# Optimization experiments

Hardware: AMD Instinct MI355X
Metric: run time of the kernel (lower is better)

Reference implementation:

```python
import jax, jax.numpy as jnp
import numpy as np
from jax import lax

N = 50000      # total nodes
E = 400000     # total edges
F = 512        # input feature dim
B = 50         # graphs in batch
NP = 1000      # nodes per graph
OUT = 10       # out_channel
EPS = 1e-5


def setup_inputs():
    key = jax.random.key(0)
    ks = jax.random.split(key, 20)
    x = jax.random.normal(ks[0], (N, F), jnp.float32)
    eg = jnp.arange(E) // (E // B)                       # graph id per edge
    src = jax.random.randint(ks[1], (E,), 0, NP) + eg * NP
    dst = jax.random.randint(ks[2], (E,), 0, NP) + eg * NP
    edge_index = jnp.stack([src, dst]).astype(jnp.int32)
    batch = (jnp.arange(N) // NP).astype(jnp.int32)
    s = 0.02
    W1 = s * jax.random.normal(ks[3], (1024, F), jnp.float32)
    b1 = jnp.zeros((1024,), jnp.float32)
    g1 = jnp.ones((1024,), jnp.float32)
    be1 = jnp.zeros((1024,), jnp.float32)
    Wp = s * jax.random.normal(ks[4], (1, 2 * 1024), jnp.float32)  # EdgePooling lin
    bp = jnp.zeros((1,), jnp.float32)
    W2 = s * jax.random.normal(ks[5], (512, 1024), jnp.float32)
    b2 = jnp.zeros((512,), jnp.float32)
    g2 = jnp.ones((512,), jnp.float32)
    be2 = jnp.zeros((512,), jnp.float32)
    Wfc = s * jax.random.normal(ks[6], (200, 512), jnp.float32)
    bfc = jnp.zeros((200,), jnp.float32)
    Wfc1 = s * jax.random.normal(ks[7], (OUT, 200), jnp.float32)
    bfc1 = jnp.zeros((OUT,), jnp.float32)
    return dict(x=x, edge_index=edge_index, batch=batch, W1=W1, b1=b1, g1=g1,
                be1=be1, Wp=Wp, bp=bp, W2=W2, b2=b2, g2=g2, be2=be2,
                Wfc=Wfc, bfc=bfc, Wfc1=Wfc1, bfc1=bfc1)


def _bn(h, g, b):
    m = h.mean(0)
    v = jnp.var(h, axis=0)  # biased var, as torch BatchNorm1d (train mode)
    return (h - m) * (g / jnp.sqrt(v + EPS)) + b


def _edge_pool(h, src, dst, batch, Wp, bp):
    # raw edge score: Linear([h_src || h_dst]) -> scalar per edge
    e = jnp.concatenate([h[src], h[dst]], axis=-1) @ Wp.T + bp  # [E,1]
    e = e[:, 0]
    # softmax over edges sharing the same destination node (PyG default)
    m = jax.ops.segment_max(e, dst, num_segments=N)
    ex = jnp.exp(e - m[dst])
    den = jax.ops.segment_sum(ex, dst, num_segments=N)
    score = ex / den[dst] + 0.5  # add_to_edge_score = 0.5

    # greedy contraction in descending-score order (sequential, like PyG)
    order = jnp.argsort(-score)
    so, do = src[order], dst[order]

    def step(merged, sd):
        s_, d_ = sd
        ok = (~merged[s_]) & (~merged[d_])
        merged = merged.at[s_].set(merged[s_] | ok)
        merged = merged.at[d_].set(merged[d_] | ok)
        return merged, ok

    _, valid = lax.scan(step, jnp.zeros(N, bool), (so, do))
    ec = (jnp.cumsum(valid.astype(jnp.int32)) - 1)      # cluster id per contracted edge
    num_merged = valid.astype(jnp.int32).sum()

    OOB = jnp.int32(N)
    cluster = jnp.full((N,), -1, jnp.int32)
    cluster = cluster.at[jnp.where(valid, so, OOB)].set(ec, mode='drop')
    cluster = cluster.at[jnp.where(valid, do, OOB)].set(ec, mode='drop')
    unmerged = cluster < 0
    rank = jnp.cumsum(unmerged.astype(jnp.int32)) - 1
    cluster = jnp.where(unmerged, num_merged + rank, cluster)

    # per-cluster multiplier: contracted-edge score, 1.0 for singleton nodes
    mult = jnp.ones((N,), h.dtype)
    mult = mult.at[jnp.where(valid, ec, OOB)].set(score[order], mode='drop')

    new_x = jax.ops.segment_sum(h, cluster, num_segments=N) * mult[:, None]
    new_batch = jnp.full((N,), B, jnp.int32).at[cluster].set(batch)  # pad slots -> dummy graph B
    return new_x, new_batch


def reference(x, edge_index, batch, W1, b1, g1, be1, Wp, bp, W2, b2, g2, be2,
              Wfc, bfc, Wfc1, bfc1):
    src, dst = edge_index[0], edge_index[1]
    # ChebConv K=1 == plain linear (only T_0 = x term)
    h = jax.nn.relu(_bn(x @ W1.T + b1, g1, be1))         # [N,1024]
    h, nb = _edge_pool(h, src, dst, batch, Wp, bp)       # [N,1024] padded, [N]
    h = jax.nn.relu(_bn(h @ W2.T + b2, g2, be2))         # [N,512]
    # global mean pool over graphs (dummy segment B holds padding)
    sums = jax.ops.segment_sum(h, nb, num_segments=B + 1)[:B]
    cnt = jax.ops.segment_sum(jnp.ones((N,), h.dtype), nb, num_segments=B + 1)[:B]
    pooled = sums / jnp.maximum(cnt, 1.0)[:, None]       # [B,512]
    hid = jax.nn.relu(pooled @ Wfc.T + bfc)              # [B,200]; dropout is eval no-op
    return hid @ Wfc1.T + bfc1                           # [B,OUT]
```

## Files before the change

### kernel.cpp

```cpp
#include <hip/hip_runtime.h>

#define Nn   50000
#define Ee   400000
#define Ff   512
#define H1   1024
#define H2   512
#define Bb   50
#define OUTd 10
#define EPSc 1e-5f
#define NPg  1000
#define EPg  8000

typedef _Float16 h8 __attribute__((ext_vector_type(8)));
typedef _Float16 h4 __attribute__((ext_vector_type(4)));
typedef float f4 __attribute__((ext_vector_type(4)));

__device__ __forceinline__ unsigned fmap(float f) {
    unsigned u = __float_as_uint(f);
    return (u & 0x80000000u) ? ~u : (u | 0x80000000u);
}
__device__ __forceinline__ float funmap(unsigned m) {
    unsigned u = (m & 0x80000000u) ? (m ^ 0x80000000u) : ~m;
    return __uint_as_float(u);
}

__device__ __forceinline__ void gl_lds16(const void* g, void* l) {
    __builtin_amdgcn_global_load_lds(
        (const __attribute__((address_space(1))) unsigned int*)g,
        (__attribute__((address_space(3))) unsigned int*)l,
        16, 0, 0);
}

__global__ void init_kernel(double* cs1, double* css1, double* cs2, double* css2, int* scal) {
    int i = blockIdx.x * blockDim.x + threadIdx.x;
    int nth = gridDim.x * blockDim.x;
    for (int j = i; j < H1; j += nth) { cs1[j] = 0.0; css1[j] = 0.0; }
    for (int j = i; j < H2; j += nth) { cs2[j] = 0.0; css2[j] = 0.0; }
    if (i < 16) scal[i] = 0;
}

__global__ void prep_kernel(const float* __restrict__ x, _Float16* __restrict__ xhi, _Float16* __restrict__ xlo,
                            const float* __restrict__ W1, _Float16* __restrict__ w1h, _Float16* __restrict__ w1l,
                            const float* __restrict__ W2, _Float16* __restrict__ w2h) {
    int i = blockIdx.x * blockDim.x + threadIdx.x;
    int nth = gridDim.x * blockDim.x;
    const int nx = Nn * Ff / 4, nw1 = H1 * Ff / 4, nw2 = H2 * H1 / 4;
    for (int k = i; k < nx; k += nth) {
        float4 v = ((const float4*)x)[k];
        h4 H = { (_Float16)v.x, (_Float16)v.y, (_Float16)v.z, (_Float16)v.w };
        h4 L = { (_Float16)(v.x - (float)H[0]), (_Float16)(v.y - (float)H[1]),
                 (_Float16)(v.z - (float)H[2]), (_Float16)(v.w - (float)H[3]) };
        ((h4*)xhi)[k] = H;
        ((h4*)xlo)[k] = L;
    }
    for (int k = i; k < nw1; k += nth) {
        float4 v = ((const float4*)W1)[k];
        h4 H = { (_Float16)v.x, (_Float16)v.y, (_Float16)v.z, (_Float16)v.w };
        h4 L = { (_Float16)(v.x - (float)H[0]), (_Float16)(v.y - (float)H[1]),
                 (_Float16)(v.z - (float)H[2]), (_Float16)(v.w - (float)H[3]) };
        ((h4*)w1h)[k] = H;
        ((h4*)w1l)[k] = L;
    }
    for (int k = i; k < nw2; k += nth) {
        float4 v = ((const float4*)W2)[k];
        h4 H = { (_Float16)v.x, (_Float16)v.y, (_Float16)v.z, (_Float16)v.w };
        ((h4*)w2h)[k] = H;
    }
}

__global__ __launch_bounds__(512) void gemm1_256_kernel(
        const _Float16* __restrict__ Ahi, const _Float16* __restrict__ Alo,
        const _Float16* __restrict__ Bhi, const _Float16* __restrict__ Blo,
        const float* __restrict__ bias, float* __restrict__ C,
        double* __restrict__ csum, double* __restrict__ cssum)
{
    const int M = Nn;
    const int nwg = gridDim.x, orig = blockIdx.x;
    const int qq = nwg >> 3, rr = nwg & 7;
    const int xcd = orig & 7, idx = orig >> 3;
    const int lin = (xcd < rr ? xcd * (qq + 1) : rr * (qq + 1) + (xcd - rr) * qq) + idx;
    const int nT = H1 / 256;
    const int bmI = lin / nT;
    const int bm = bmI * 256, bn = (lin - bmI * nT) * 256;
    __shared__ __align__(16) _Float16 smem[2][2][256 * 32];
    const int tid = threadIdx.x, lane = tid & 63, wave = tid >> 6;
    const int rIn = lane >> 2;
    const int kSrcByte = ((((lane & 3) - ((lane >> 3) & 3)) & 3) << 4);
    const int wr = wave >> 2, wc = wave & 3;
    const int lr = lane & 15, kb = lane >> 4;
    const int pGr = ((kb + ((lr >> 1) & 3)) & 3) << 3;
    const int sArr = wave >> 2;
    const int sQtr = wave & 3;
    const _Float16* sGp = sArr ? Alo : Ahi;
    f4 acc[8][4] = {};

    auto STAGE = [&](int b, int k0) {
        _Float16* lp = smem[b][sArr] + sQtr * (64 * 32);
#pragma unroll
        for (int c2 = 0; c2 < 4; ++c2) {
            int row = min(bm + sQtr * 64 + c2 * 16 + rIn, M - 1);
            gl_lds16((const char*)sGp + ((size_t)row * Ff + k0) * 2 + kSrcByte, lp + c2 * 512);
        }
    };

    int cur = 0;
    STAGE(0, 0);
    for (int k0 = 0; k0 < Ff; k0 += 32) {
        __syncthreads();
        if (k0 + 32 < Ff) STAGE(cur ^ 1, k0 + 32);
        const _Float16* AhP = smem[cur][0];
        const _Float16* AlP = smem[cur][1];
        h8 ahf[8], alf[8];
#pragma unroll
        for (int mi = 0; mi < 8; ++mi) {
            const int ar = (wr * 128 + mi * 16 + lr) * 32 + pGr;
            ahf[mi] = *(const h8*)&AhP[ar];
            alf[mi] = *(const h8*)&AlP[ar];
        }
#pragma unroll
        for (int ni = 0; ni < 4; ++ni) {
            const size_t boff = (size_t)(bn + wc * 64 + ni * 16 + lr) * Ff + k0 + kb * 8;
            const h8 bh = *(const h8*)&Bhi[boff];
            const h8 bl = *(const h8*)&Blo[boff];
#pragma unroll
            for (int mi = 0; mi < 8; ++mi) {
                acc[mi][ni] = __builtin_amdgcn_mfma_f32_16x16x32_f16(ahf[mi], bh, acc[mi][ni], 0, 0, 0);
                acc[mi][ni] = __builtin_amdgcn_mfma_f32_16x16x32_f16(ahf[mi], bl, acc[mi][ni], 0, 0, 0);
                acc[mi][ni] = __builtin_amdgcn_mfma_f32_16x16x32_f16(alf[mi], bh, acc[mi][ni], 0, 0, 0);
            }
        }
        cur ^= 1;
    }
#pragma unroll
    for (int ni = 0; ni < 4; ++ni) {
        const int col = bn + wc * 64 + ni * 16 + lr;
        const float bv = bias[col];
        double sd_ = 0.0, ssd = 0.0;
#pragma unroll
        for (int mi = 0; mi < 8; ++mi)
#pragma unroll
            for (int r = 0; r < 4; ++r) {
                int row = bm + wr * 128 + mi * 16 + kb * 4 + r;
                if (row < M) {
                    float v = acc[mi][ni][r] + bv;
                    C[(size_t)row * H1 + col] = v;
                    sd_ += (double)v;
                    ssd += (double)v * (double)v;
                }
            }
        sd_ += __shfl_xor(sd_, 16); ssd += __shfl_xor(ssd, 16);
        sd_ += __shfl_xor(sd_, 32); ssd += __shfl_xor(ssd, 32);
        if (kb == 0) {
            atomicAdd(&csum[col], sd_);
            atomicAdd(&cssum[col], ssd);
        }
    }
}

__global__ __launch_bounds__(256) void gemm2_kernel(
        const _Float16* __restrict__ Ag, const _Float16* __restrict__ Bh,
        const float* __restrict__ bias, float* __restrict__ C,
        const int* __restrict__ Mptr, int nT,
        double* __restrict__ csum, double* __restrict__ cssum)
{
    const int M = Mptr[0];
    const int nwg = gridDim.x, orig = blockIdx.x;
    const int qq = nwg >> 3, rr = nwg & 7;
    const int xcd = orig & 7, idx = orig >> 3;
    const int lin = (xcd < rr ? xcd * (qq + 1) : rr * (qq + 1) + (xcd - rr) * qq) + idx;
    const int bmI = lin / nT;
    const int bm = bmI * 128, bn = (lin - bmI * nT) * 128;
    if (bm >= M) return;
    __shared__ __align__(16) _Float16 smem[2][128 * 32];
    const int tid = threadIdx.x, lane = tid & 63, wave = tid >> 6;
    const int rIn = lane >> 2;
    const int kSrcByte = ((((lane & 3) - ((lane >> 3) & 3)) & 3) << 4);
    const int wr = wave >> 1, wc = wave & 1;
    const int lr = lane & 15, kb = lane >> 4;
    const int pGr = ((kb + ((lr >> 1) & 3)) & 3) << 3;
    f4 acc[4][4] = {};

    auto STAGE = [&](int b, int k0) {
        _Float16* lp = smem[b] + wave * (32 * 32);
#pragma unroll
        for (int c2 = 0; c2 < 2; ++c2) {
            int row = min(bm + wave * 32 + c2 * 16 + rIn, M - 1);
            gl_lds16((const char*)Ag + ((size_t)row * H1 + k0) * 2 + kSrcByte, lp + c2 * 512);
        }
    };

    int cur = 0;
    STAGE(0, 0);
    for (int k0 = 0; k0 < H1; k0 += 32) {
        __syncthreads();
        if (k0 + 32 < H1) STAGE(cur ^ 1, k0 + 32);
        const _Float16* AhP = smem[cur];
        h8 ahf[4];
#pragma unroll
        for (int mi = 0; mi < 4; ++mi)
            ahf[mi] = *(const h8*)&AhP[(wr * 64 + mi * 16 + lr) * 32 + pGr];
#pragma unroll
        for (int ni = 0; ni < 4; ++ni) {
            const h8 bh = *(const h8*)&Bh[(size_t)(bn + wc * 64 + ni * 16 + lr) * H1 + k0 + kb * 8];
#pragma unroll
            for (int mi = 0; mi < 4; ++mi)
                acc[mi][ni] = __builtin_amdgcn_mfma_f32_16x16x32_f16(ahf[mi], bh, acc[mi][ni], 0, 0, 0);
        }
        cur ^= 1;
    }
#pragma unroll
    for (int ni = 0; ni < 4; ++ni) {
        const int col = bn + wc * 64 + ni * 16 + lr;
        const float bv = bias[col];
        double sd_ = 0.0, ssd = 0.0;
#pragma unroll
        for (int mi = 0; mi < 4; ++mi)
#pragma unroll
            for (int r = 0; r < 4; ++r) {
                int row = bm + wr * 64 + mi * 16 + kb * 4 + r;
                if (row < M) {
                    float v = acc[mi][ni][r] + bv;
                    C[(size_t)row * H2 + col] = v;
                    sd_ += (double)v;
                    ssd += (double)v * (double)v;
                }
            }
        sd_ += __shfl_xor(sd_, 16); ssd += __shfl_xor(ssd, 16);
        sd_ += __shfl_xor(sd_, 32); ssd += __shfl_xor(ssd, 32);
        if (kb == 0) {
            atomicAdd(&csum[col], sd_);
            atomicAdd(&cssum[col], ssd);
        }
    }
}

__global__ void bnparam_kernel(const double* __restrict__ s, const double* __restrict__ ss,
                               const float* __restrict__ g, const float* __restrict__ be,
                               float* __restrict__ a, float* __restrict__ bb, int cols,
                               const float* __restrict__ padBias, const int* __restrict__ CvPtr) {
    int j = blockIdx.x * blockDim.x + threadIdx.x;
    if (j >= cols) return;
    double sum = s[j], sumsq = ss[j];
    if (CvPtr) {
        double pad = (double)(Nn - CvPtr[0]);
        double bv = padBias ? (double)padBias[j] : 0.0;
        sum += pad * bv; sumsq += pad * bv * bv;
    }
    double mean = sum / (double)Nn;
    double var = sumsq / (double)Nn - mean * mean;
    float aj = g[j] / sqrtf((float)var + EPSc);
    a[j] = aj;
    bb[j] = be[j] - (float)mean * aj;
}

__global__ __launch_bounds__(256) void pq_kernel(const float* __restrict__ h,
        const float* __restrict__ a, const float* __restrict__ bb,
        const float* __restrict__ Wp, float* __restrict__ p, float* __restrict__ q) {
    const int n = blockIdx.x * 4 + (threadIdx.x >> 6);
    if (n >= Nn) return;
    const int lane = threadIdx.x & 63;
    float sp = 0.f, sq = 0.f;
    const float* row = h + (size_t)n * H1;
#pragma unroll
    for (int u = 0; u < 4; ++u) {
        int j = u * 256 + lane * 4;
        float4 v = *(const float4*)(row + j);
        const float4 av = *(const float4*)(a + j);
        const float4 bv = *(const float4*)(bb + j);
        v.x = fmaxf(v.x * av.x + bv.x, 0.f);
        v.y = fmaxf(v.y * av.y + bv.y, 0.f);
        v.z = fmaxf(v.z * av.z + bv.z, 0.f);
        v.w = fmaxf(v.w * av.w + bv.w, 0.f);
        const float4 wp = *(const float4*)(Wp + j);
        const float4 wq = *(const float4*)(Wp + H1 + j);
        sp += v.x * wp.x + v.y * wp.y + v.z * wp.z + v.w * wp.w;
        sq += v.x * wq.x + v.y * wq.y + v.z * wq.z + v.w * wq.w;
    }
#pragma unroll
    for (int off = 32; off > 0; off >>= 1) {
        sp += __shfl_xor(sp, off);
        sq += __shfl_xor(sq, off);
    }
    if (lane == 0) { p[n] = sp; q[n] = sq; }
}

__global__ __launch_bounds__(1024) void match_fused_kernel(
        const int* __restrict__ ei,
        const float* __restrict__ p, const float* __restrict__ q,
        const float* __restrict__ bp,
        unsigned long long* __restrict__ packed,
        int* __restrict__ nodeA, int* __restrict__ nodeB,
        float* __restrict__ multc, int* __restrict__ scal,
        int* __restrict__ gbase, int* __restrict__ gcnt) {
    __shared__ __align__(16) char LB[52096];
    unsigned short* lst = (unsigned short*)LB;
    float* earr = (float*)LB;
    float* pl = (float*)(LB + 32000);
    float* ql = pl + NPg;
    unsigned long long* best = (unsigned long long*)(LB + 32000);
    unsigned* maxu = (unsigned*)(LB + 40000);
    int* mergedS = (int*)(LB + 40000);
    unsigned long long* den = (unsigned long long*)(LB + 44000);
    float* lmult = (float*)(LB + 44000);
    unsigned short* lsA = (unsigned short*)(LB + 48000);
    unsigned short* ldA = (unsigned short*)(LB + 50000);
    int* cnts = (int*)(LB + 52032);

    const int g = blockIdx.x;
    const int tid = threadIdx.x;
    const int e0 = g * EPg, n0 = g * NPg;
    const int* srcp = ei + e0;
    const int* dstp = ei + Ee + e0;
    const float bpv = bp[0];

    for (int i = tid; i < NPg; i += 1024) {
        pl[i] = p[n0 + i];
        ql[i] = q[n0 + i];
        maxu[i] = 0u;
        den[i] = 0ull;
    }
    __syncthreads();
    for (int i = tid; i < EPg; i += 1024) {
        int s = srcp[i] - n0, d = dstp[i] - n0;
        float e = pl[s] + ql[d] + bpv;
        earr[i] = e;
        atomicMax(&maxu[d], fmap(e));
    }
    __syncthreads();
    for (int i = tid; i < EPg; i += 1024) {
        int d = dstp[i] - n0;
        float ex = expf(earr[i] - funmap(maxu[d]));
        atomicAdd(&den[d], (unsigned long long)(ex * 4294967296.0f));
    }
    __syncthreads();
    for (int i = tid; i < EPg; i += 1024) {
        int s = srcp[i] - n0, d = dstp[i] - n0;
        float ex = expf(earr[i] - funmap(maxu[d]));
        float den_f = (float)((double)den[d] * (1.0 / 4294967296.0));
        float sc = ex / den_f + 0.5f;
        packed[e0 + i] = ((unsigned long long)__float_as_uint(sc) << 33)
                       | ((unsigned long long)(8191u - (unsigned)i) << 20)
                       | ((unsigned long long)(unsigned)s << 10) | (unsigned long long)(unsigned)d;
    }
    __syncthreads();
    for (int i = tid; i < NPg; i += 1024) mergedS[i] = 0;
    for (int i = tid; i < EPg; i += 1024) lst[i] = (unsigned short)i;
    if (tid == 0) { cnts[0] = EPg; cnts[1] = 0; cnts[2] = 0; }
    __syncthreads();
    int cur = 0;
    for (int round = 0; round < 20000; ++round) {
        const int n_cur = cnts[cur];
        if (n_cur == 0) break;
        if (tid == 0) cnts[cur ^ 1] = 0;
        for (int i = tid; i < NPg; i += 1024) best[i] = 0ull;
        __syncthreads();
        for (int ii = tid; ii < n_cur; ii += 1024) {
            int le = lst[cur * EPg + ii];
            unsigned long long pk = packed[e0 + le];
            int s = (int)((pk >> 10) & 1023), d = (int)(pk & 1023);
            if (mergedS[s] | mergedS[d]) { lst[cur * EPg + ii] = 0xFFFF; continue; }
            atomicMax(&best[s], pk);
            atomicMax(&best[d], pk);
        }
        __syncthreads();
        for (int ii = tid; ii < n_cur; ii += 1024) {
            int le = lst[cur * EPg + ii];
            if (le == 0xFFFF) continue;
            unsigned long long pk = packed[e0 + le];
            int s = (int)((pk >> 10) & 1023), d = (int)(pk & 1023);
            if (best[s] == pk && best[d] == pk) {
                int c = atomicAdd(&cnts[2], 1);
                lsA[c] = (unsigned short)s;
                ldA[c] = (s == d) ? (unsigned short)0xFFFF : (unsigned short)d;
                lmult[c] = __uint_as_float((unsigned)(pk >> 33));
                mergedS[s] = 1;
                if (d != s) mergedS[d] = 1;
            } else {
                int pos = atomicAdd(&cnts[cur ^ 1], 1);
                lst[(cur ^ 1) * EPg + pos] = (unsigned short)le;
            }
        }
        __syncthreads();
        cur ^= 1;
    }
    for (int i = tid; i < NPg; i += 1024) {
        if (!mergedS[i]) {
            int c = atomicAdd(&cnts[2], 1);
            lsA[c] = (unsigned short)i;
            ldA[c] = 0xFFFF;
            lmult[c] = 1.0f;
        }
    }
    __syncthreads();
    if (tid == 0) {
        int ncl = cnts[2];
        int base = atomicAdd(&scal[2], ncl);
        cnts[3] = base;
        gbase[g] = base;
        gcnt[g] = ncl;
    }
    __syncthreads();
    const int ncl = cnts[2], base = cnts[3];
    for (int i = tid; i < ncl; i += 1024) {
        nodeA[base + i] = n0 + (int)lsA[i];
        nodeB[base + i] = (ldA[i] == 0xFFFF) ? -1 : (n0 + (int)ldA[i]);
        multc[base + i] = lmult[i];
    }
}

__global__ __launch_bounds__(256) void gather_kernel(const float* __restrict__ h,
        const float* __restrict__ a, const float* __restrict__ bb,
        const int* __restrict__ nodeA, const int* __restrict__ nodeB,
        const float* __restrict__ multc, const int* __restrict__ scal,
        _Float16* __restrict__ Ag) {
    int c = blockIdx.x * 4 + (threadIdx.x >> 6);
    if (c >= scal[2]) return;
    const int lane = threadIdx.x & 63;
    int na = nodeA[c], nb = nodeB[c];
    float mu = multc[c];
#pragma unroll
    for (int u = 0; u < 4; ++u) {
        int j = u * 256 + lane * 4;
        const float4 av = *(const float4*)(a + j);
        const float4 bv = *(const float4*)(bb + j);
        float4 v = *(const float4*)(h + (size_t)na * H1 + j);
        v.x = fmaxf(v.x * av.x + bv.x, 0.f);
        v.y = fmaxf(v.y * av.y + bv.y, 0.f);
        v.z = fmaxf(v.z * av.z + bv.z, 0.f);
        v.w = fmaxf(v.w * av.w + bv.w, 0.f);
        if (nb >= 0) {
            float4 w = *(const float4*)(h + (size_t)nb * H1 + j);
            v.x += fmaxf(w.x * av.x + bv.x, 0.f);
            v.y += fmaxf(w.y * av.y + bv.y, 0.f);
            v.z += fmaxf(w.z * av.z + bv.z, 0.f);
            v.w += fmaxf(w.w * av.w + bv.w, 0.f);
        }
        h4 o = { (_Float16)(mu * v.x), (_Float16)(mu * v.y), (_Float16)(mu * v.z), (_Float16)(mu * v.w) };
        *(h4*)(Ag + (size_t)c * H1 + j) = o;
    }
}

__global__ __launch_bounds__(256) void pool_seg_kernel(const float* __restrict__ C2,
        const float* __restrict__ a2, const float* __restrict__ bb2,
        const int* __restrict__ gbase, const int* __restrict__ gcnt,
        float* __restrict__ pool) {
    const int g = blockIdx.x;
    const int j = blockIdx.y * 256 + threadIdx.x;
    const int b0 = gbase[g], cN = gcnt[g];
    const float aj = a2[j], bj = bb2[j];
    float s = 0.f;
    for (int c = b0; c < b0 + cN; ++c)
        s += fmaxf(C2[(size_t)c * H2 + j] * aj + bj, 0.f);
    pool[g * H2 + j] = s;
}

__global__ void fc1_kernel(const float* __restrict__ pool, const int* __restrict__ gcnt,
                           const float* __restrict__ Wfc, const float* __restrict__ bfc,
                           float* __restrict__ hid) {
    int g = blockIdx.x;
    int o = threadIdx.x;
    float inv = 1.0f / fmaxf((float)gcnt[g], 1.0f);
    if (o < 200) {
        float s = 0.f;
        for (int j = 0; j < H2; ++j) s += (pool[g * H2 + j] * inv) * Wfc[o * H2 + j];
        hid[g * 200 + o] = fmaxf(s + bfc[o], 0.f);
    }
}
__global__ void fc2_kernel(const float* __restrict__ hid, const float* __restrict__ Wfc1,
                           const float* __restrict__ bfc1, float* __restrict__ out) {
    int idx = threadIdx.x;
    if (idx < Bb * OUTd) {
        int g = idx / OUTd, o = idx % OUTd;
        float s = bfc1[o];
        for (int t = 0; t < 200; ++t) s += hid[g * 200 + t] * Wfc1[o * 200 + t];
        out[idx] = s;
    }
}

extern "C" void kernel_launch(void* const* d_in, const int* in_sizes, int n_in,
                              void* d_out, int out_size, void* d_ws, size_t ws_size,
                              hipStream_t stream) {
    (void)in_sizes; (void)n_in; (void)out_size; (void)ws_size;
    const float* x    = (const float*)d_in[0];
    const int*   ei   = (const int*)d_in[1];
    const float* W1   = (const float*)d_in[3];
    const float* b1   = (const float*)d_in[4];
    const float* g1   = (const float*)d_in[5];
    const float* be1  = (const float*)d_in[6];
    const float* Wp   = (const float*)d_in[7];
    const float* bp   = (const float*)d_in[8];
    const float* W2   = (const float*)d_in[9];
    const float* b2   = (const float*)d_in[10];
    const float* g2   = (const float*)d_in[11];
    const float* be2  = (const float*)d_in[12];
    const float* Wfc  = (const float*)d_in[13];
    const float* bfc  = (const float*)d_in[14];
    const float* Wfc1 = (const float*)d_in[15];
    const float* bfc1 = (const float*)d_in[16];

    char* w = (char*)d_ws;
    auto take = [&](size_t bytes) -> char* {
        char* r = w;
        w += (bytes + 255) & ~(size_t)255;
        return r;
    };
    float* h      = (float*)take((size_t)Nn * H1 * 4);
    _Float16* xhi = (_Float16*)take((size_t)Nn * Ff * 2);
    _Float16* xlo = (_Float16*)take((size_t)Nn * Ff * 2);
    _Float16* w1h = (_Float16*)take((size_t)H1 * Ff * 2);
    _Float16* w1l = (_Float16*)take((size_t)H1 * Ff * 2);
    _Float16* w2h = (_Float16*)take((size_t)H2 * H1 * 2);
    float* p      = (float*)take((size_t)Nn * 4);
    float* q      = (float*)take((size_t)Nn * 4);
    unsigned long long* packed = (unsigned long long*)take((size_t)Ee * 8);
    int* nodeA    = (int*)take((size_t)Nn * 4);
    int* nodeB    = (int*)take((size_t)Nn * 4);
    float* multc  = (float*)take((size_t)Nn * 4);
    double* cs1   = (double*)take((size_t)H1 * 8);
    double* css1  = (double*)take((size_t)H1 * 8);
    double* cs2   = (double*)take((size_t)H2 * 8);
    double* css2  = (double*)take((size_t)H2 * 8);
    float* a1     = (float*)take((size_t)H1 * 4);
    float* bb1    = (float*)take((size_t)H1 * 4);
    float* a2     = (float*)take((size_t)H2 * 4);
    float* bb2    = (float*)take((size_t)H2 * 4);
    float* pool   = (float*)take((size_t)Bb * H2 * 4);
    float* hid    = (float*)take((size_t)Bb * 200 * 4);
    int* scal     = (int*)take(64 * 4);
    int* gbase    = (int*)take(64 * 4);
    int* gcnt     = (int*)take(64 * 4);
    _Float16* Ag  = xhi;
    float* C2o    = h;

    const int mT  = (Nn + 127) / 128;
    const int mT2 = (Nn + 255) / 256;

    init_kernel<<<dim3(16), dim3(256), 0, stream>>>(cs1, css1, cs2, css2, scal);
    prep_kernel<<<dim3(2048), dim3(256), 0, stream>>>(x, xhi, xlo, W1, w1h, w1l, W2, w2h);
    gemm1_256_kernel<<<dim3(mT2 * (H1 / 256)), dim3(512), 0, stream>>>(
        xhi, xlo, w1h, w1l, b1, h, cs1, css1);
    bnparam_kernel<<<dim3((H1 + 255) / 256), dim3(256), 0, stream>>>(cs1, css1, g1, be1, a1, bb1, H1, (const float*)nullptr, (const int*)nullptr);
    pq_kernel<<<dim3((Nn + 3) / 4), dim3(256), 0, stream>>>(h, a1, bb1, Wp, p, q);
    match_fused_kernel<<<dim3(Bb), dim3(1024), 0, stream>>>(ei, p, q, bp, packed,
        nodeA, nodeB, multc, scal, gbase, gcnt);
    gather_kernel<<<dim3((Nn + 3) / 4), dim3(256), 0, stream>>>(h, a1, bb1, nodeA, nodeB, multc, scal, Ag);
    gemm2_kernel<<<dim3(mT * (H2 / 128)), dim3(256), 0, stream>>>(
        Ag, w2h, b2, C2o, scal + 2, H2 / 128, cs2, css2);
    bnparam_kernel<<<dim3((H2 + 255) / 256), dim3(256), 0, stream>>>(cs2, css2, g2, be2, a2, bb2, H2, b2, scal + 2);
    pool_seg_kernel<<<dim3(Bb, H2 / 256), dim3(256), 0, stream>>>(C2o, a2, bb2, gbase, gcnt, pool);
    fc1_kernel<<<dim3(Bb), dim3(256), 0, stream>>>(pool, gcnt, Wfc, bfc, hid);
    fc2_kernel<<<dim3(1), dim3(512), 0, stream>>>(hid, Wfc1, bfc1, (float*)d_out);
}
```

Measured before the change: 795.5 us.

## Stage B operand tiles in LDS for both GEMMs and fuse init into prep

Both GEMM kernels now load the weight (B) tiles into shared memory through async global-to-LDS copies, using the same swizzled layout as the A tiles. Previously every wave read B fragments straight from global memory, once per k-step. This cuts redundant global traffic and latency stalls inside the MFMA loop. The cost is more LDS: gemm1 goes to 128KB of shared memory, which may reduce occupancy. The accumulator-zeroing init kernel is also folded into prep_kernel, saving one launch.

Result: faster. 666.8 us (-16.2%).

```diff
diff --git a/kernel.cpp b/kernel.cpp
--- a/kernel.cpp
+++ b/kernel.cpp
@@ -31,19 +31,16 @@
         16, 0, 0);
 }
 
-__global__ void init_kernel(double* cs1, double* css1, double* cs2, double* css2, int* scal) {
+__global__ void prep_kernel(const float* __restrict__ x, _Float16* __restrict__ xhi, _Float16* __restrict__ xlo,
+                            const float* __restrict__ W1, _Float16* __restrict__ w1h, _Float16* __restrict__ w1l,
+                            const float* __restrict__ W2, _Float16* __restrict__ w2h,
+                            double* __restrict__ cs1, double* __restrict__ css1,
+                            double* __restrict__ cs2, double* __restrict__ css2, int* __restrict__ scal) {
     int i = blockIdx.x * blockDim.x + threadIdx.x;
     int nth = gridDim.x * blockDim.x;
     for (int j = i; j < H1; j += nth) { cs1[j] = 0.0; css1[j] = 0.0; }
     for (int j = i; j < H2; j += nth) { cs2[j] = 0.0; css2[j] = 0.0; }
     if (i < 16) scal[i] = 0;
-}
-
-__global__ void prep_kernel(const float* __restrict__ x, _Float16* __restrict__ xhi, _Float16* __restrict__ xlo,
-                            const float* __restrict__ W1, _Float16* __restrict__ w1h, _Float16* __restrict__ w1l,
-                            const float* __restrict__ W2, _Float16* __restrict__ w2h) {
-    int i = blockIdx.x * blockDim.x + threadIdx.x;
-    int nth = gridDim.x * blockDim.x;
     const int nx = Nn * Ff / 4, nw1 = H1 * Ff / 4, nw2 = H2 * H1 / 4;
     for (int k = i; k < nx; k += nth) {
         float4 v = ((const float4*)x)[k];
@@ -82,24 +79,27 @@
     const int nT = H1 / 256;
     const int bmI = lin / nT;
     const int bm = bmI * 256, bn = (lin - bmI * nT) * 256;
-    __shared__ __align__(16) _Float16 smem[2][2][256 * 32];
+    __shared__ __align__(16) _Float16 smem[2][4][256 * 32];
     const int tid = threadIdx.x, lane = tid & 63, wave = tid >> 6;
     const int rIn = lane >> 2;
     const int kSrcByte = ((((lane & 3) - ((lane >> 3) & 3)) & 3) << 4);
     const int wr = wave >> 2, wc = wave & 3;
     const int lr = lane & 15, kb = lane >> 4;
     const int pGr = ((kb + ((lr >> 1) & 3)) & 3) << 3;
-    const int sArr = wave >> 2;
-    const int sQtr = wave & 3;
-    const _Float16* sGp = sArr ? Alo : Ahi;
+    const int arr = wave >> 1;
+    const int hv = wave & 1;
+    const bool isA = (arr < 2);
+    const _Float16* gp = (arr == 0) ? Ahi : (arr == 1) ? Alo : (arr == 2) ? Bhi : Blo;
+    const int tb = isA ? bm : bn;
     f4 acc[8][4] = {};
 
     auto STAGE = [&](int b, int k0) {
-        _Float16* lp = smem[b][sArr] + sQtr * (64 * 32);
-#pragma unroll
-        for (int c2 = 0; c2 < 4; ++c2) {
-            int row = min(bm + sQtr * 64 + c2 * 16 + rIn, M - 1);
-            gl_lds16((const char*)sGp + ((size_t)row * Ff + k0) * 2 + kSrcByte, lp + c2 * 512);
+        _Float16* lp = smem[b][arr] + hv * (128 * 32);
+#pragma unroll
+        for (int c = 0; c < 8; ++c) {
+            int row = tb + hv * 128 + c * 16 + rIn;
+            if (isA) row = min(row, M - 1);
+            gl_lds16((const char*)gp + ((size_t)row * Ff + k0) * 2 + kSrcByte, lp + c * 512);
         }
     };
 
@@ -110,6 +110,8 @@
         if (k0 + 32 < Ff) STAGE(cur ^ 1, k0 + 32);
         const _Float16* AhP = smem[cur][0];
         const _Float16* AlP = smem[cur][1];
+        const _Float16* BhP = smem[cur][2];
+        const _Float16* BlP = smem[cur][3];
         h8 ahf[8], alf[8];
 #pragma unroll
         for (int mi = 0; mi < 8; ++mi) {
@@ -119,9 +121,9 @@
         }
 #pragma unroll
         for (int ni = 0; ni < 4; ++ni) {
-            const size_t boff = (size_t)(bn + wc * 64 + ni * 16 + lr) * Ff + k0 + kb * 8;
-            const h8 bh = *(const h8*)&Bhi[boff];
-            const h8 bl = *(const h8*)&Blo[boff];
+            const int br = (wc * 64 + ni * 16 + lr) * 32 + pGr;
+            const h8 bh = *(const h8*)&BhP[br];
+            const h8 bl = *(const h8*)&BlP[br];
 #pragma unroll
             for (int mi = 0; mi < 8; ++mi) {
                 acc[mi][ni] = __builtin_amdgcn_mfma_f32_16x16x32_f16(ahf[mi], bh, acc[mi][ni], 0, 0, 0);
@@ -171,7 +173,7 @@
     const int bmI = lin / nT;
     const int bm = bmI * 128, bn = (lin - bmI * nT) * 128;
     if (bm >= M) return;
-    __shared__ __align__(16) _Float16 smem[2][128 * 32];
+    __shared__ __align__(16) _Float16 smem[2][2][128 * 32];
     const int tid = threadIdx.x, lane = tid & 63, wave = tid >> 6;
     const int rIn = lane >> 2;
     const int kSrcByte = ((((lane & 3) - ((lane >> 3) & 3)) & 3) << 4);
@@ -181,11 +183,17 @@
     f4 acc[4][4] = {};
 
     auto STAGE = [&](int b, int k0) {
-        _Float16* lp = smem[b] + wave * (32 * 32);
-#pragma unroll
-        for (int c2 = 0; c2 < 2; ++c2) {
-            int row = min(bm + wave * 32 + c2 * 16 + rIn, M - 1);
-            gl_lds16((const char*)Ag + ((size_t)row * H1 + k0) * 2 + kSrcByte, lp + c2 * 512);
+        const bool isA = (wave < 2);
+        const _Float16* gp = isA ? Ag : Bh;
+        _Float16* lp = smem[b][isA ? 0 : 1];
+        const int tb = isA ? bm : bn;
+        const int hf = wave & 1;
+#pragma unroll
+        for (int c2 = 0; c2 < 4; ++c2) {
+            int c = hf * 4 + c2;
+            int row = tb + c * 16 + rIn;
+            if (isA) row = min(row, M - 1);
+            gl_lds16((const char*)gp + ((size_t)row * H1 + k0) * 2 + kSrcByte, lp + c * 512);
         }
     };
 
@@ -194,18 +202,21 @@
     for (int k0 = 0; k0 < H1; k0 += 32) {
         __syncthreads();
         if (k0 + 32 < H1) STAGE(cur ^ 1, k0 + 32);
-        const _Float16* AhP = smem[cur];
-        h8 ahf[4];
+        const _Float16* AhP = smem[cur][0];
+        const _Float16* BhP = smem[cur][1];
+        const int ar = (wr * 64 + lr) * 32 + pGr;
+        const int br = (wc * 64 + lr) * 32 + pGr;
+        h8 ahf[4], bhf[4];
+#pragma unroll
+        for (int i = 0; i < 4; ++i) {
+            ahf[i] = *(const h8*)&AhP[ar + i * 512];
+            bhf[i] = *(const h8*)&BhP[br + i * 512];
+        }
 #pragma unroll
         for (int mi = 0; mi < 4; ++mi)
-            ahf[mi] = *(const h8*)&AhP[(wr * 64 + mi * 16 + lr) * 32 + pGr];
-#pragma unroll
-        for (int ni = 0; ni < 4; ++ni) {
-            const h8 bh = *(const h8*)&Bh[(size_t)(bn + wc * 64 + ni * 16 + lr) * H1 + k0 + kb * 8];
-#pragma unroll
-            for (int mi = 0; mi < 4; ++mi)
-                acc[mi][ni] = __builtin_amdgcn_mfma_f32_16x16x32_f16(ahf[mi], bh, acc[mi][ni], 0, 0, 0);
-        }
+#pragma unroll
+            for (int ni = 0; ni < 4; ++ni)
+                acc[mi][ni] = __builtin_amdgcn_mfma_f32_16x16x32_f16(ahf[mi], bhf[ni], acc[mi][ni], 0, 0, 0);
         cur ^= 1;
     }
 #pragma unroll
@@ -535,8 +546,8 @@
     const int mT  = (Nn + 127) / 128;
     const int mT2 = (Nn + 255) / 256;
 
-    init_kernel<<<dim3(16), dim3(256), 0, stream>>>(cs1, css1, cs2, css2, scal);
-    prep_kernel<<<dim3(2048), dim3(256), 0, stream>>>(x, xhi, xlo, W1, w1h, w1l, W2, w2h);
+    prep_kernel<<<dim3(2048), dim3(256), 0, stream>>>(x, xhi, xlo, W1, w1h, w1l, W2, w2h,
+                                                      cs1, css1, cs2, css2, scal);
     gemm1_256_kernel<<<dim3(mT2 * (H1 / 256)), dim3(512), 0, stream>>>(
         xhi, xlo, w1h, w1l, b1, h, cs1, css1);
     bnparam_kernel<<<dim3((H1 + 255) / 256), dim3(256), 0, stream>>>(cs1, css1, g1, be1, a1, bb1, H1, (const float*)nullptr, (const int*)nullptr);
```
